# Optimization experiments

Hardware: AMD Instinct MI355X
Metric: run time of the kernel (lower is better)

## Reference

```python
import jax, jax.numpy as jnp
import numpy as np
import math

H, D, E, KD = 8, 128, 128, 16      # n_heads, input_dim, embed_dim, key_dim=val_dim
B, NPICK, NDEL = 16, 250, 250      # batch, pickups, deliveries per instance
G = 1 + NPICK + NDEL               # depot + picks + deliveries


def setup_inputs() -> dict:
    key = jax.random.key(0)
    ks = jax.random.split(key, 10)
    sk = 1.0 / math.sqrt(KD)
    se = 1.0 / math.sqrt(E)
    u = lambda k, shp, s: jax.random.uniform(k, shp, jnp.float32, -s, s)
    return {
        "q": jax.random.normal(ks[0], (B, G, D), jnp.float32),
        "W_query": u(ks[1], (H, D, KD), sk),
        "W_key": u(ks[2], (H, D, KD), sk),
        "W_val": u(ks[3], (H, D, KD), sk),
        "W1_query": u(ks[4], (H, D, KD), sk),
        "W2_query": u(ks[5], (H, D, KD), sk),
        "W3_query": u(ks[6], (H, D, KD), sk),
        "W4_query": u(ks[7], (H, D, KD), sk),
        "W_out": u(ks[8], (H, KD, E), se),
        "n_pick": NPICK,
        "n_delivery": NDEL,
    }


def reference(q, W_query, W_key, W_val, W1_query, W2_query, W3_query, W4_query,
              W_out, n_pick, n_delivery):
    h = q                                   # self-attention (h is None in caller)
    Bq, Gq, Dq = h.shape
    nh = W_query.shape[0]
    kd = W_query.shape[2]
    nf = 1.0 / math.sqrt(kd)
    NEG = jnp.float32(-jnp.inf)

    proj = lambda x, W: jnp.einsum('bnd,hdk->hbnk', x, W)   # (H,B,N,kd)
    scores = lambda Q, K: nf * jnp.einsum('hbqk,hbgk->hbqg', Q, K)
    # torch masked_fill_(x==0, -inf) on the group blocks (padding sentinel)
    zmask = lambda c: jnp.where(c == 0, NEG, c)

    Q = proj(q, W_query)
    K = proj(h, W_key)
    V = proj(h, W_val)
    comp = scores(Q, K)                      # (H,B,G,G)

    # split_embeddings: depot at 0, picks 1..n_pick, deliveries at the end
    hp = h[:, 1:1 + n_pick]                  # (B, n_pick, D)
    hd = h[:, 1 + n_pick:]                   # (B, n_delivery, D)

    Kp, Vp = proj(hp, W_key), proj(hp, W_val)
    Kd, Vd = proj(hd, W_key), proj(hd, W_val)

    c_pp = zmask(scores(proj(hp, W1_query), Kp))  # pick  -> all picks
    c_pd = zmask(scores(proj(hp, W2_query), Kd))  # pick  -> all deliveries
    c_dp = zmask(scores(proj(hd, W3_query), Kp))  # deliv -> all picks
    c_dd = zmask(scores(proj(hd, W4_query), Kd))  # deliv -> all deliveries

    def place(block, row_start):
        # scatter block rows into a (H,B,G,cols) tensor filled with -inf
        full = jnp.full((nh, Bq, Gq, block.shape[3]), NEG, dtype=block.dtype)
        return full.at[:, :, row_start:row_start + block.shape[2], :].set(block)

    add_pp = place(c_pp, 1)
    add_pd = place(c_pd, 1)
    add_dd = place(c_dd, Gq - n_delivery)
    add_dp = place(c_dp, Gq - n_delivery)

    comp_full = jnp.concatenate([comp, add_pp, add_pd, add_dd, add_dp], axis=-1)
    attn = jax.nn.softmax(comp_full, axis=-1)

    g, mp, md = Gq, n_pick, n_delivery
    heads = jnp.einsum('hbqg,hbgv->hbqv', attn[..., :g], V)
    heads = heads + jnp.einsum('hbqp,hbpv->hbqv', attn[..., g:g + mp], Vp)
    heads = heads + jnp.einsum('hbqd,hbdv->hbqv', attn[..., g + mp:g + mp + md], Vd)
    heads = heads + jnp.einsum('hbqd,hbdv->hbqv', attn[..., g + mp + md:g + mp + 2 * md], Vd)
    heads = heads + jnp.einsum('hbqp,hbpv->hbqv', attn[..., g + mp + 2 * md:g + 2 * mp + 2 * md], Vp)

    out = jnp.einsum('hbqv,hve->bqe', heads, W_out)   # (B, G, E)
    return out
```

## Files before the change

### kernel.cpp

```cpp
#include <hip/hip_runtime.h>
#include <math.h>

#define NH 8
#define DIM 128
#define KD 16
#define NB 16
#define NG 501
#define NPK 250
#define QROWS 512
#define QSCALE 0.36067376022224085f

typedef unsigned short ushort_t;
typedef __attribute__((ext_vector_type(8))) short short8v;
typedef __attribute__((ext_vector_type(4))) short short4v;
typedef __attribute__((ext_vector_type(2))) short short2v;
typedef __attribute__((ext_vector_type(4))) float f32x4;

#define MFMA(a, b, c) __builtin_amdgcn_mfma_f32_16x16x32_bf16(a, b, c, 0, 0, 0)

static __device__ __forceinline__ ushort_t f2bf(float x) {
  union { float f; unsigned u; } v; v.f = x;
  unsigned r = v.u + 0x7FFFu + ((v.u >> 16) & 1u);
  return (ushort_t)(r >> 16);
}
static __device__ __forceinline__ float bf2f(ushort_t h) {
  union { unsigned u; float f; } v; v.u = ((unsigned)h) << 16;
  return v.f;
}
static __device__ __forceinline__ unsigned cvtpk(float lo, float hi) {
  unsigned r;
  asm("v_cvt_pk_bf16_f32 %0, %1, %2" : "=v"(r) : "v"(lo), "v"(hi));
  return r;
}

__global__ __launch_bounds__(256) void conv_kernel(
    const float* __restrict__ q, ushort_t* __restrict__ qh,
    ushort_t* __restrict__ ql)
{
  int idx = blockIdx.x * 256 + threadIdx.x;
  int b  = idx >> 13;
  int r  = (idx >> 4) & 511;
  int c8 = (idx & 15) * 8;
  short8v h8 = {0,0,0,0,0,0,0,0}, l8 = {0,0,0,0,0,0,0,0};
  if (r < NG) {
    const float* src = &q[(size_t)(b * NG + r) * DIM + c8];
    float4 a = *(const float4*)src, d = *(const float4*)(src + 4);
    float vals[8] = {a.x, a.y, a.z, a.w, d.x, d.y, d.z, d.w};
#pragma unroll
    for (int j = 0; j < 8; ++j) {
      ushort_t hi = f2bf(vals[j]);
      h8[j] = (short)hi;
      l8[j] = (short)f2bf(vals[j] - bf2f(hi));
    }
  }
  size_t off = (size_t)(b * 512 + r) * DIM + c8;
  *(short8v*)&qh[off] = h8;
  *(short8v*)&ql[off] = l8;
}

__global__ __launch_bounds__(256) void proj_kernel(
    const ushort_t* __restrict__ qh_g, const ushort_t* __restrict__ ql_g,
    const float* __restrict__ wq, const float* __restrict__ wk,
    const float* __restrict__ wv, const float* __restrict__ w1,
    const float* __restrict__ w2, const float* __restrict__ w3,
    const float* __restrict__ w4,
    ushort_t* __restrict__ QcH, ushort_t* __restrict__ QcL,
    ushort_t* __restrict__ QPH, ushort_t* __restrict__ QPL,
    ushort_t* __restrict__ QDH, ushort_t* __restrict__ QDL,
    ushort_t* __restrict__ Kb,  ushort_t* __restrict__ Vt)
{
  const int rc = blockIdx.x, b = blockIdx.y, h = blockIdx.z;
  const int tid = threadIdx.x;
  const int wid = tid >> 6, lane = tid & 63;
  const int lrow = lane & 15, kgrp = lane >> 4;
  const size_t hb = (size_t)h * NB + b;

  const float* Wptr[7] = {wq, wk, wv, w1, w2, w3, w4};
  const int p0 = wid * 2;
  const int p1 = (wid < 3) ? wid * 2 + 1 : -1;

  short8v whf[2][4], wlf[2][4];
#pragma unroll
  for (int slot = 0; slot < 2; ++slot) {
    int p = slot ? p1 : p0;
    if (p < 0) continue;
    const float* W = Wptr[p] + h * 2048 + lrow;
#pragma unroll
    for (int c = 0; c < 4; ++c) {
      short8v hh, ll;
#pragma unroll
      for (int j = 0; j < 8; ++j) {
        float v = W[(c * 32 + kgrp * 8 + j) * 16];
        ushort_t hi = f2bf(v);
        hh[j] = (short)hi;
        ll[j] = (short)f2bf(v - bf2f(hi));
      }
      whf[slot][c] = hh; wlf[slot][c] = ll;
    }
  }

  const f32x4 zero4 = {0.f, 0.f, 0.f, 0.f};

#pragma unroll 1
  for (int iter = 0; iter < 2; ++iter) {
    const int rowbase = rc * 64 + iter * 32;
    short8v qhf[2][4], qlf[2][4];
#pragma unroll
    for (int s = 0; s < 2; ++s)
#pragma unroll
      for (int c = 0; c < 4; ++c) {
        size_t off = (size_t)(b * 512 + rowbase + s * 16 + lrow) * DIM + c * 32 + kgrp * 8;
        qhf[s][c] = *(const short8v*)(qh_g + off);
        qlf[s][c] = *(const short8v*)(ql_g + off);
      }

    f32x4 acc[2][2] = {{zero4, zero4}, {zero4, zero4}};
#pragma unroll
    for (int c = 0; c < 4; ++c)
#pragma unroll
      for (int slot = 0; slot < 2; ++slot) {
        int p = slot ? p1 : p0;
        if (p < 0) continue;
#pragma unroll
        for (int s = 0; s < 2; ++s) {
          if (p == 2) {
            acc[slot][s] = MFMA(whf[slot][c], qlf[s][c], acc[slot][s]);
            acc[slot][s] = MFMA(wlf[slot][c], qhf[s][c], acc[slot][s]);
            acc[slot][s] = MFMA(whf[slot][c], qhf[s][c], acc[slot][s]);
          } else {
            acc[slot][s] = MFMA(qlf[s][c], whf[slot][c], acc[slot][s]);
            acc[slot][s] = MFMA(qhf[s][c], wlf[slot][c], acc[slot][s]);
            acc[slot][s] = MFMA(qhf[s][c], whf[slot][c], acc[slot][s]);
          }
        }
      }

#pragma unroll
    for (int slot = 0; slot < 2; ++slot) {
      int p = slot ? p1 : p0;
      if (p < 0) continue;
#pragma unroll
      for (int s = 0; s < 2; ++s) {
#pragma unroll
        for (int rg = 0; rg < 4; ++rg) {
          float x = acc[slot][s][rg];
          if (p == 2) {
            int v = kgrp * 4 + rg;
            int g = rowbase + s * 16 + lrow;
            Vt[hb * 8192 + (size_t)v * 512 + g] = f2bf(x);
          } else {
            int row = rowbase + s * 16 + kgrp * 4 + rg;
            if (p == 0) {
              float xs = x * QSCALE;
              ushort_t hi = f2bf(xs), lo = f2bf(xs - bf2f(hi));
              size_t off = hb * 8192 + (size_t)row * 16 + lrow;
              QcH[off] = hi; QcL[off] = lo;
            } else if (p == 1) {
              ushort_t hi = f2bf(x), lo = f2bf(x - bf2f(hi));
              size_t off = hb * 16384 + (size_t)row * 32 + lrow;
              Kb[off] = hi; Kb[off + 16] = lo;
            } else {
              bool lowr = (p == 3 || p == 4);
              bool write = lowr ? (row <= NPK) : (row > NPK);
              if (write) {
                float xs = (row == 0) ? 0.f : x * QSCALE;
                ushort_t hi = f2bf(xs), lo = f2bf(xs - bf2f(hi));
                ushort_t* dH = (p == 3 || p == 5) ? QPH : QDH;
                ushort_t* dL = (p == 3 || p == 5) ? QPL : QDL;
                size_t off = hb * 8192 + (size_t)row * 16 + lrow;
                dH[off] = hi; dL[off] = lo;
              }
            }
          }
        }
      }
    }
  }
}

__global__ __launch_bounds__(256, 2) void attn_kernel(
    const ushort_t* __restrict__ QcH, const ushort_t* __restrict__ QcL,
    const ushort_t* __restrict__ QPH, const ushort_t* __restrict__ QPL,
    const ushort_t* __restrict__ QDH, const ushort_t* __restrict__ QDL,
    const ushort_t* __restrict__ Kb,  const ushort_t* __restrict__ Vt,
    ushort_t* __restrict__ HdH, ushort_t* __restrict__ HdL)
{
  __shared__ __align__(16) ushort_t Klds[16384];
  __shared__ __align__(16) ushort_t Vlds[8192];

  const int rt = blockIdx.x, b = blockIdx.y, h = blockIdx.z;
  const int tid = threadIdx.x;
  const int wid = tid >> 6, lane = tid & 63;
  const int lhalf = lane >> 4, lcol = lane & 15;
  const size_t hb = (size_t)h * NB + b;

  const ushort_t* Kg = Kb + hb * (size_t)(QROWS * 32);
  for (int c = tid; c < 2048; c += 256)
    *(short8v*)&Klds[c * 8] = *(const short8v*)(Kg + (size_t)c * 8);

  const ushort_t* Vg = Vt + hb * (size_t)(16 * QROWS);
#pragma unroll
  for (int it = 0; it < 4; ++it) {
    int c = it * 256 + tid;
    int blk = (it * 16) + (c & 15);
    int v = (c >> 4) & 15;
    int grp = blk >> 2, lh = blk & 3;
    short8v val = *(const short8v*)(Vg + (size_t)v * QROWS + blk * 8);
    *(short8v*)&Vlds[((grp * 4 + lh) * 16 + v) * 8] = val;
  }
  __syncthreads();

  const int wrow = rt * 128 + wid * 32;
  short8v qch[2], qcl[2], qph[2], qpl[2], qdh[2], qdl[2];
#pragma unroll
  for (int f = 0; f < 2; ++f) {
    int row = wrow + f * 16 + lcol;
    size_t off = hb * (size_t)(QROWS * 16) + (size_t)row * 16;
    size_t offh = off + (lhalf & 1) * 8;
    qch[f] = *(const short8v*)(QcH + offh);
    qph[f] = *(const short8v*)(QPH + offh);
    qdh[f] = *(const short8v*)(QDH + offh);
    short8v zl = {0,0,0,0,0,0,0,0};
    qcl[f] = zl; qpl[f] = zl; qdl[f] = zl;
    if (lhalf < 2) {
      size_t offl = off + lhalf * 8;
      qcl[f] = *(const short8v*)(QcL + offl);
      qpl[f] = *(const short8v*)(QPL + offl);
      qdl[f] = *(const short8v*)(QDL + offl);
    }
  }

  const f32x4 zero4 = {0.f, 0.f, 0.f, 0.f};
  f32x4 Oacc[2] = {zero4, zero4};
  float lsum[2] = {0.f, 0.f};
  const int srcA = ((lhalf & 1) * 2) * 16 + lcol;
  const int srcB = srcA + 16;
  const bool selhi = (lhalf >= 2);

#pragma unroll 1
  for (int grp = 0; grp < 16; ++grp) {
    float pv[2][2][4];
#pragma unroll
    for (int half = 0; half < 2; ++half) {
      const int ch = grp * 2 + half;
      short8v ka = *(const short8v*)&Klds[((ch * 16 + lcol) * 4 + lhalf) * 8];
#pragma unroll
      for (int qf = 0; qf < 2; ++qf) {
        f32x4 sc = MFMA(ka, qcl[qf], zero4);
        sc = MFMA(ka, qch[qf], sc);
        f32x4 se;
        if (ch == 15) {
          f32x4 sp = MFMA(ka, qpl[qf], zero4); sp = MFMA(ka, qph[qf], sp);
          f32x4 sd = MFMA(ka, qdl[qf], zero4); sd = MFMA(ka, qdh[qf], sd);
#pragma unroll
          for (int rg = 0; rg < 4; ++rg) {
            int key = 240 + lhalf * 4 + rg;
            se[rg] = (key <= NPK) ? sp[rg] : sd[rg];
          }
        } else if (ch <= 14) {
          se = MFMA(ka, qpl[qf], zero4); se = MFMA(ka, qph[qf], se);
        } else {
          se = MFMA(ka, qdl[qf], zero4); se = MFMA(ka, qdh[qf], se);
        }
#pragma unroll
        for (int rg = 0; rg < 4; ++rg) {
          float ec = __builtin_amdgcn_exp2f(sc[rg]);
          float ee = (se[rg] == 0.0f) ? 0.0f : __builtin_amdgcn_exp2f(se[rg]);
          if (ch == 0 && rg == 0) ee = (lhalf == 0) ? 0.0f : ee;
          float pt = ec + ee;
          if (ch == 31) pt = (lhalf * 4 + rg <= 4) ? pt : 0.0f;
          lsum[qf] += pt;
          pv[half][qf][rg] = pt;
        }
      }
    }
#pragma unroll
    for (int qf = 0; qf < 2; ++qf) {
      unsigned a0 = cvtpk(pv[0][qf][0], pv[0][qf][1]);
      unsigned a1 = cvtpk(pv[0][qf][2], pv[0][qf][3]);
      unsigned b0 = cvtpk(pv[1][qf][0], pv[1][qf][1]);
      unsigned b1 = cvtpk(pv[1][qf][2], pv[1][qf][3]);
      unsigned h0A = (unsigned)__shfl((int)a0, srcA);
      unsigned h0B = (unsigned)__shfl((int)a1, srcA);
      unsigned h0C = (unsigned)__shfl((int)a0, srcB);
      unsigned h0D = (unsigned)__shfl((int)a1, srcB);
      unsigned h1A = (unsigned)__shfl((int)b0, srcA);
      unsigned h1B = (unsigned)__shfl((int)b1, srcA);
      unsigned h1C = (unsigned)__shfl((int)b0, srcB);
      unsigned h1D = (unsigned)__shfl((int)b1, srcB);
      union { unsigned u[4]; short8v s; } pb;
      pb.u[0] = selhi ? h1A : h0A;
      pb.u[1] = selhi ? h1B : h0B;
      pb.u[2] = selhi ? h1C : h0C;
      pb.u[3] = selhi ? h1D : h0D;
      short8v va = *(const short8v*)&Vlds[((grp * 4 + lhalf) * 16 + lcol) * 8];
      Oacc[qf] = MFMA(va, pb.s, Oacc[qf]);
    }
  }

#pragma unroll
  for (int qf = 0; qf < 2; ++qf) {
    float l = lsum[qf];
    l += __shfl_xor(l, 16);
    l += __shfl_xor(l, 32);
    float inv = 1.0f / l;
    int row = wrow + qf * 16 + lcol;
    if (row < NG) {
      short4v ph, pl;
#pragma unroll
      for (int rg = 0; rg < 4; ++rg) {
        float o = Oacc[qf][rg] * inv;
        ushort_t hi = f2bf(o);
        ph[rg] = (short)hi;
        pl[rg] = (short)f2bf(o - bf2f(hi));
      }
      size_t off = (hb * 512 + (size_t)row) * 16 + lhalf * 4;
      *(short4v*)&HdH[off] = ph;
      *(short4v*)&HdL[off] = pl;
    }
  }
}

__global__ __launch_bounds__(256) void out_kernel(
    const ushort_t* __restrict__ HdH, const ushort_t* __restrict__ HdL,
    const float* __restrict__ Wout, float* __restrict__ out)
{
  const int eh = blockIdx.x, rt = blockIdx.y, b = blockIdx.z;
  const int tid = threadIdx.x;
  const int wid = tid >> 6, lane = tid & 63;
  const int lrow = lane & 15, kgrp = lane >> 4;
  const int e0 = eh * 64 + wid * 16 + lrow;

  short8v bh[4], bl[4];
#pragma unroll
  for (int c = 0; c < 4; ++c) {
    short8v hh, ll;
#pragma unroll
    for (int j = 0; j < 8; ++j) {
      float v = Wout[(size_t)(c * 32 + kgrp * 8 + j) * 128 + e0];
      ushort_t hi = f2bf(v);
      hh[j] = (short)hi;
      ll[j] = (short)f2bf(v - bf2f(hi));
    }
    bh[c] = hh; bl[c] = ll;
  }

  short8v ah[2][4], al[2][4];
#pragma unroll
  for (int s = 0; s < 2; ++s)
#pragma unroll
    for (int c = 0; c < 4; ++c) {
      int hh = (c * 4 + kgrp) >> 1, kd0 = ((c * 4 + kgrp) & 1) * 8;
      size_t off = ((size_t)(hh * NB + b) * 512 + rt * 32 + s * 16 + lrow) * 16 + kd0;
      ah[s][c] = *(const short8v*)(HdH + off);
      al[s][c] = *(const short8v*)(HdL + off);
    }

  const f32x4 zero4 = {0.f, 0.f, 0.f, 0.f};
  f32x4 acc[2] = {zero4, zero4};
#pragma unroll
  for (int c = 0; c < 4; ++c)
#pragma unroll
    for (int s = 0; s < 2; ++s) {
      acc[s] = MFMA(al[s][c], bh[c], acc[s]);
      acc[s] = MFMA(ah[s][c], bl[c], acc[s]);
      acc[s] = MFMA(ah[s][c], bh[c], acc[s]);
    }

#pragma unroll
  for (int s = 0; s < 2; ++s)
#pragma unroll
    for (int rg = 0; rg < 4; ++rg) {
      int g = rt * 32 + s * 16 + kgrp * 4 + rg;
      if (g < NG) out[((size_t)b * NG + g) * 128 + e0] = acc[s][rg];
    }
}

extern "C" void kernel_launch(void* const* d_in, const int* in_sizes, int n_in,
                              void* d_out, int out_size, void* d_ws, size_t ws_size,
                              hipStream_t stream)
{
  const float* q  = (const float*)d_in[0];
  const float* Wq = (const float*)d_in[1];
  const float* Wk = (const float*)d_in[2];
  const float* Wv = (const float*)d_in[3];
  const float* W1 = (const float*)d_in[4];
  const float* W2 = (const float*)d_in[5];
  const float* W3 = (const float*)d_in[6];
  const float* W4 = (const float*)d_in[7];
  const float* Wo = (const float*)d_in[8];
  float* out = (float*)d_out;

  char* wsb = (char*)d_ws;
  ushort_t* qh_g = (ushort_t*)(wsb + (0u  << 20));
  ushort_t* ql_g = (ushort_t*)(wsb + (2u  << 20));
  ushort_t* QcH  = (ushort_t*)(wsb + (4u  << 20));
  ushort_t* QcL  = (ushort_t*)(wsb + (6u  << 20));
  ushort_t* QPH  = (ushort_t*)(wsb + (8u  << 20));
  ushort_t* QPL  = (ushort_t*)(wsb + (10u << 20));
  ushort_t* QDH  = (ushort_t*)(wsb + (12u << 20));
  ushort_t* QDL  = (ushort_t*)(wsb + (14u << 20));
  ushort_t* Kb   = (ushort_t*)(wsb + (16u << 20));
  ushort_t* Vt   = (ushort_t*)(wsb + (20u << 20));
  ushort_t* HdH  = qh_g;
  ushort_t* HdL  = ql_g;

  conv_kernel<<<dim3(512), 256, 0, stream>>>(q, qh_g, ql_g);
  proj_kernel<<<dim3(8, NB, NH), 256, 0, stream>>>(qh_g, ql_g,
                                                   Wq, Wk, Wv, W1, W2, W3, W4,
                                                   QcH, QcL, QPH, QPL, QDH, QDL, Kb, Vt);
  attn_kernel<<<dim3(4, NB, NH), 256, 0, stream>>>(QcH, QcL, QPH, QPL, QDH, QDL,
                                                   Kb, Vt, HdH, HdL);
  out_kernel<<<dim3(2, 16, NB), 256, 0, stream>>>(HdH, HdL, Wo, out);
}
```

Baseline: 129.9 us.

## Pre-split weights once in conv kernel; shrink per-wave work in attn and out kernels

Moves the fp32-to-bf16 hi/lo splitting of all projection and output weights into the conversion kernel, writing them once in MFMA fragment layout instead of redoing the split in every proj and out block. The proj kernel now streams weights and q fragments per k-chunk to lower register pressure and raise occupancy. The attention kernel switches to 512-thread blocks where each wave handles 16 rows instead of 32, and the out kernel launches twice as many blocks with half the rows each. The aim is more parallelism and less redundant conversion, at the cost of extra workspace traffic and more K/V LDS loads per row.

```diff
diff --git a/kernel.cpp b/kernel.cpp
--- a/kernel.cpp
+++ b/kernel.cpp
@@ -13,7 +13,6 @@
 typedef unsigned short ushort_t;
 typedef __attribute__((ext_vector_type(8))) short short8v;
 typedef __attribute__((ext_vector_type(4))) short short4v;
-typedef __attribute__((ext_vector_type(2))) short short2v;
 typedef __attribute__((ext_vector_type(4))) float f32x4;
 
 #define MFMA(a, b, c) __builtin_amdgcn_mfma_f32_16x16x32_bf16(a, b, c, 0, 0, 0)
@@ -33,37 +32,61 @@
   return r;
 }
 
+
 __global__ __launch_bounds__(256) void conv_kernel(
-    const float* __restrict__ q, ushort_t* __restrict__ qh,
-    ushort_t* __restrict__ ql)
-{
-  int idx = blockIdx.x * 256 + threadIdx.x;
-  int b  = idx >> 13;
-  int r  = (idx >> 4) & 511;
-  int c8 = (idx & 15) * 8;
-  short8v h8 = {0,0,0,0,0,0,0,0}, l8 = {0,0,0,0,0,0,0,0};
-  if (r < NG) {
-    const float* src = &q[(size_t)(b * NG + r) * DIM + c8];
-    float4 a = *(const float4*)src, d = *(const float4*)(src + 4);
-    float vals[8] = {a.x, a.y, a.z, a.w, d.x, d.y, d.z, d.w};
-#pragma unroll
-    for (int j = 0; j < 8; ++j) {
-      ushort_t hi = f2bf(vals[j]);
-      h8[j] = (short)hi;
-      l8[j] = (short)f2bf(vals[j] - bf2f(hi));
-    }
-  }
-  size_t off = (size_t)(b * 512 + r) * DIM + c8;
-  *(short8v*)&qh[off] = h8;
-  *(short8v*)&ql[off] = l8;
-}
-
-__global__ __launch_bounds__(256) void proj_kernel(
-    const ushort_t* __restrict__ qh_g, const ushort_t* __restrict__ ql_g,
+    const float* __restrict__ q,
     const float* __restrict__ wq, const float* __restrict__ wk,
     const float* __restrict__ wv, const float* __restrict__ w1,
     const float* __restrict__ w2, const float* __restrict__ w3,
-    const float* __restrict__ w4,
+    const float* __restrict__ w4, const float* __restrict__ wo,
+    ushort_t* __restrict__ qh_g, ushort_t* __restrict__ ql_g,
+    ushort_t* __restrict__ Wsh,  ushort_t* __restrict__ Wsl,
+    ushort_t* __restrict__ Wosh, ushort_t* __restrict__ Wosl)
+{
+  const int idx = blockIdx.x * 256 + threadIdx.x;
+  {
+    int b = idx >> 13, r = (idx >> 4) & 511, c8 = (idx & 15) * 8;
+    short8v h8 = {0,0,0,0,0,0,0,0}, l8 = {0,0,0,0,0,0,0,0};
+    if (r < NG) {
+      const float* src = &q[(size_t)(b * NG + r) * DIM + c8];
+      float4 x = *(const float4*)src, y = *(const float4*)(src + 4);
+      float vals[8] = {x.x, x.y, x.z, x.w, y.x, y.y, y.z, y.w};
+#pragma unroll
+      for (int j = 0; j < 8; ++j) {
+        ushort_t hi = f2bf(vals[j]);
+        h8[j] = (short)hi;
+        l8[j] = (short)f2bf(vals[j] - bf2f(hi));
+      }
+    }
+    size_t off = (size_t)(b * 512 + r) * DIM + c8;
+    *(short8v*)&qh_g[off] = h8;
+    *(short8v*)&ql_g[off] = l8;
+  }
+  if (idx < 114688) {
+    int p = idx >> 14, rem = idx & 16383;
+    int h = rem >> 11, r2 = rem & 2047;
+    int d = r2 >> 4, lrow = r2 & 15;
+    const float* W = (p == 0) ? wq : (p == 1) ? wk : (p == 2) ? wv :
+                     (p == 3) ? w1 : (p == 4) ? w2 : (p == 5) ? w3 : w4;
+    float v = W[h * 2048 + d * 16 + lrow];
+    ushort_t hi = f2bf(v), lo = f2bf(v - bf2f(hi));
+    int c = d >> 5, kg = (d >> 3) & 3, j = d & 7;
+    size_t dst = ((((size_t)(p * 8 + h) * 4 + c) * 4 + kg) * 16 + lrow) * 8 + j;
+    Wsh[dst] = hi; Wsl[dst] = lo;
+  }
+  if (idx < 16384) {
+    int hkd = idx >> 7, e = idx & 127;
+    float v = wo[(size_t)hkd * 128 + e];
+    ushort_t hi = f2bf(v), lo = f2bf(v - bf2f(hi));
+    int c = hkd >> 5, kg = (hkd >> 3) & 3, j = hkd & 7;
+    size_t dst = (((size_t)c * 4 + kg) * 128 + e) * 8 + j;
+    Wosh[dst] = hi; Wosl[dst] = lo;
+  }
+}
+
+__global__ __launch_bounds__(256, 4) void proj_kernel(
+    const ushort_t* __restrict__ qh_g, const ushort_t* __restrict__ ql_g,
+    const ushort_t* __restrict__ Wsh,  const ushort_t* __restrict__ Wsl,
     ushort_t* __restrict__ QcH, ushort_t* __restrict__ QcL,
     ushort_t* __restrict__ QPH, ushort_t* __restrict__ QPL,
     ushort_t* __restrict__ QDH, ushort_t* __restrict__ QDL,
@@ -74,66 +97,46 @@
   const int wid = tid >> 6, lane = tid & 63;
   const int lrow = lane & 15, kgrp = lane >> 4;
   const size_t hb = (size_t)h * NB + b;
-
-  const float* Wptr[7] = {wq, wk, wv, w1, w2, w3, w4};
   const int p0 = wid * 2;
   const int p1 = (wid < 3) ? wid * 2 + 1 : -1;
-
-  short8v whf[2][4], wlf[2][4];
-#pragma unroll
-  for (int slot = 0; slot < 2; ++slot) {
-    int p = slot ? p1 : p0;
-    if (p < 0) continue;
-    const float* W = Wptr[p] + h * 2048 + lrow;
-#pragma unroll
-    for (int c = 0; c < 4; ++c) {
-      short8v hh, ll;
-#pragma unroll
-      for (int j = 0; j < 8; ++j) {
-        float v = W[(c * 32 + kgrp * 8 + j) * 16];
-        ushort_t hi = f2bf(v);
-        hh[j] = (short)hi;
-        ll[j] = (short)f2bf(v - bf2f(hi));
-      }
-      whf[slot][c] = hh; wlf[slot][c] = ll;
-    }
-  }
-
   const f32x4 zero4 = {0.f, 0.f, 0.f, 0.f};
 
 #pragma unroll 1
   for (int iter = 0; iter < 2; ++iter) {
     const int rowbase = rc * 64 + iter * 32;
-    short8v qhf[2][4], qlf[2][4];
-#pragma unroll
-    for (int s = 0; s < 2; ++s)
-#pragma unroll
-      for (int c = 0; c < 4; ++c) {
-        size_t off = (size_t)(b * 512 + rowbase + s * 16 + lrow) * DIM + c * 32 + kgrp * 8;
-        qhf[s][c] = *(const short8v*)(qh_g + off);
-        qlf[s][c] = *(const short8v*)(ql_g + off);
-      }
-
     f32x4 acc[2][2] = {{zero4, zero4}, {zero4, zero4}};
 #pragma unroll
-    for (int c = 0; c < 4; ++c)
+    for (int c = 0; c < 4; ++c) {
+      size_t qoff0 = (size_t)(b * 512 + rowbase + lrow) * DIM + c * 32 + kgrp * 8;
+      size_t qoff1 = qoff0 + 16 * DIM;
+      short8v qh0 = *(const short8v*)(qh_g + qoff0);
+      short8v ql0 = *(const short8v*)(ql_g + qoff0);
+      short8v qh1 = *(const short8v*)(qh_g + qoff1);
+      short8v ql1 = *(const short8v*)(ql_g + qoff1);
 #pragma unroll
       for (int slot = 0; slot < 2; ++slot) {
         int p = slot ? p1 : p0;
         if (p < 0) continue;
-#pragma unroll
-        for (int s = 0; s < 2; ++s) {
-          if (p == 2) {
-            acc[slot][s] = MFMA(whf[slot][c], qlf[s][c], acc[slot][s]);
-            acc[slot][s] = MFMA(wlf[slot][c], qhf[s][c], acc[slot][s]);
-            acc[slot][s] = MFMA(whf[slot][c], qhf[s][c], acc[slot][s]);
-          } else {
-            acc[slot][s] = MFMA(qlf[s][c], whf[slot][c], acc[slot][s]);
-            acc[slot][s] = MFMA(qhf[s][c], wlf[slot][c], acc[slot][s]);
-            acc[slot][s] = MFMA(qhf[s][c], whf[slot][c], acc[slot][s]);
-          }
+        size_t woff = ((((size_t)(p * 8 + h) * 4 + c) * 4 + kgrp) * 16 + lrow) * 8;
+        short8v wh = *(const short8v*)&Wsh[woff];
+        short8v wl = *(const short8v*)&Wsl[woff];
+        if (p == 2) {
+          acc[slot][0] = MFMA(wh, ql0, acc[slot][0]);
+          acc[slot][0] = MFMA(wl, qh0, acc[slot][0]);
+          acc[slot][0] = MFMA(wh, qh0, acc[slot][0]);
+          acc[slot][1] = MFMA(wh, ql1, acc[slot][1]);
+          acc[slot][1] = MFMA(wl, qh1, acc[slot][1]);
+          acc[slot][1] = MFMA(wh, qh1, acc[slot][1]);
+        } else {
+          acc[slot][0] = MFMA(ql0, wh, acc[slot][0]);
+          acc[slot][0] = MFMA(qh0, wl, acc[slot][0]);
+          acc[slot][0] = MFMA(qh0, wh, acc[slot][0]);
+          acc[slot][1] = MFMA(ql1, wh, acc[slot][1]);
+          acc[slot][1] = MFMA(qh1, wl, acc[slot][1]);
+          acc[slot][1] = MFMA(qh1, wh, acc[slot][1]);
         }
       }
+    }
 
 #pragma unroll
     for (int slot = 0; slot < 2; ++slot) {
@@ -178,7 +181,7 @@
   }
 }
 
-__global__ __launch_bounds__(256, 2) void attn_kernel(
+__global__ __launch_bounds__(512, 4) void attn_kernel(
     const ushort_t* __restrict__ QcH, const ushort_t* __restrict__ QcL,
     const ushort_t* __restrict__ QPH, const ushort_t* __restrict__ QPL,
     const ushort_t* __restrict__ QDH, const ushort_t* __restrict__ QDL,
@@ -194,186 +197,159 @@
   const int lhalf = lane >> 4, lcol = lane & 15;
   const size_t hb = (size_t)h * NB + b;
 
+  const int wrow = rt * 128 + wid * 16;
+  const int row = wrow + lcol;
+  size_t off = hb * (size_t)(QROWS * 16) + (size_t)row * 16;
+  size_t offh = off + (lhalf & 1) * 8;
+  short8v qch = *(const short8v*)(QcH + offh);
+  short8v qph = *(const short8v*)(QPH + offh);
+  short8v qdh = *(const short8v*)(QDH + offh);
+  short8v qcl = {0,0,0,0,0,0,0,0}, qpl = qcl, qdl = qcl;
+  if (lhalf < 2) {
+    size_t offl = off + lhalf * 8;
+    qcl = *(const short8v*)(QcL + offl);
+    qpl = *(const short8v*)(QPL + offl);
+    qdl = *(const short8v*)(QDL + offl);
+  }
+
   const ushort_t* Kg = Kb + hb * (size_t)(QROWS * 32);
-  for (int c = tid; c < 2048; c += 256)
+  for (int c = tid; c < 2048; c += 512)
     *(short8v*)&Klds[c * 8] = *(const short8v*)(Kg + (size_t)c * 8);
-
   const ushort_t* Vg = Vt + hb * (size_t)(16 * QROWS);
 #pragma unroll
-  for (int it = 0; it < 4; ++it) {
-    int c = it * 256 + tid;
-    int blk = (it * 16) + (c & 15);
-    int v = (c >> 4) & 15;
-    int grp = blk >> 2, lh = blk & 3;
+  for (int it = 0; it < 2; ++it) {
+    int i = it * 512 + tid;
+    int v = (i >> 4) & 15;
+    int blk = (i >> 8) * 16 + (i & 15);
+    int g2 = blk >> 2, lh = blk & 3;
     short8v val = *(const short8v*)(Vg + (size_t)v * QROWS + blk * 8);
-    *(short8v*)&Vlds[((grp * 4 + lh) * 16 + v) * 8] = val;
+    *(short8v*)&Vlds[((g2 * 4 + lh) * 16 + v) * 8] = val;
   }
   __syncthreads();
 
-  const int wrow = rt * 128 + wid * 32;
-  short8v qch[2], qcl[2], qph[2], qpl[2], qdh[2], qdl[2];
-#pragma unroll
-  for (int f = 0; f < 2; ++f) {
-    int row = wrow + f * 16 + lcol;
-    size_t off = hb * (size_t)(QROWS * 16) + (size_t)row * 16;
-    size_t offh = off + (lhalf & 1) * 8;
-    qch[f] = *(const short8v*)(QcH + offh);
-    qph[f] = *(const short8v*)(QPH + offh);
-    qdh[f] = *(const short8v*)(QDH + offh);
-    short8v zl = {0,0,0,0,0,0,0,0};
-    qcl[f] = zl; qpl[f] = zl; qdl[f] = zl;
-    if (lhalf < 2) {
-      size_t offl = off + lhalf * 8;
-      qcl[f] = *(const short8v*)(QcL + offl);
-      qpl[f] = *(const short8v*)(QPL + offl);
-      qdl[f] = *(const short8v*)(QDL + offl);
-    }
-  }
-
   const f32x4 zero4 = {0.f, 0.f, 0.f, 0.f};
-  f32x4 Oacc[2] = {zero4, zero4};
-  float lsum[2] = {0.f, 0.f};
+  f32x4 Oacc = zero4;
+  float lsum = 0.f;
   const int srcA = ((lhalf & 1) * 2) * 16 + lcol;
   const int srcB = srcA + 16;
   const bool selhi = (lhalf >= 2);
 
 #pragma unroll 1
   for (int grp = 0; grp < 16; ++grp) {
-    float pv[2][2][4];
+    const int ch0 = grp * 2, ch1 = ch0 + 1;
+    short8v ka0 = *(const short8v*)&Klds[((ch0 * 16 + lcol) * 4 + lhalf) * 8];
+    short8v ka1 = *(const short8v*)&Klds[((ch1 * 16 + lcol) * 4 + lhalf) * 8];
+    short8v va  = *(const short8v*)&Vlds[((grp * 4 + lhalf) * 16 + lcol) * 8];
+
+    float pv[2][4];
 #pragma unroll
     for (int half = 0; half < 2; ++half) {
-      const int ch = grp * 2 + half;
-      short8v ka = *(const short8v*)&Klds[((ch * 16 + lcol) * 4 + lhalf) * 8];
-#pragma unroll
-      for (int qf = 0; qf < 2; ++qf) {
-        f32x4 sc = MFMA(ka, qcl[qf], zero4);
-        sc = MFMA(ka, qch[qf], sc);
-        f32x4 se;
-        if (ch == 15) {
-          f32x4 sp = MFMA(ka, qpl[qf], zero4); sp = MFMA(ka, qph[qf], sp);
-          f32x4 sd = MFMA(ka, qdl[qf], zero4); sd = MFMA(ka, qdh[qf], sd);
-#pragma unroll
-          for (int rg = 0; rg < 4; ++rg) {
-            int key = 240 + lhalf * 4 + rg;
-            se[rg] = (key <= NPK) ? sp[rg] : sd[rg];
-          }
-        } else if (ch <= 14) {
-          se = MFMA(ka, qpl[qf], zero4); se = MFMA(ka, qph[qf], se);
-        } else {
-          se = MFMA(ka, qdl[qf], zero4); se = MFMA(ka, qdh[qf], se);
+      const int ch = ch0 + half;
+      short8v ka = half ? ka1 : ka0;
+      f32x4 sc = MFMA(ka, qcl, zero4);
+      sc = MFMA(ka, qch, sc);
+      f32x4 se;
+      if (ch == 15) {
+        f32x4 sp = MFMA(ka, qpl, zero4); sp = MFMA(ka, qph, sp);
+        f32x4 sd = MFMA(ka, qdl, zero4); sd = MFMA(ka, qdh, sd);
+#pragma unroll
+        for (int rg = 0; rg < 4; ++rg) {
+          int key = 240 + lhalf * 4 + rg;
+          se[rg] = (key <= NPK) ? sp[rg] : sd[rg];
         }
-#pragma unroll
-        for (int rg = 0; rg < 4; ++rg) {
-          float ec = __builtin_amdgcn_exp2f(sc[rg]);
-          float ee = (se[rg] == 0.0f) ? 0.0f : __builtin_amdgcn_exp2f(se[rg]);
-          if (ch == 0 && rg == 0) ee = (lhalf == 0) ? 0.0f : ee;
-          float pt = ec + ee;
-          if (ch == 31) pt = (lhalf * 4 + rg <= 4) ? pt : 0.0f;
-          lsum[qf] += pt;
-          pv[half][qf][rg] = pt;
-        }
-      }
-    }
-#pragma unroll
-    for (int qf = 0; qf < 2; ++qf) {
-      unsigned a0 = cvtpk(pv[0][qf][0], pv[0][qf][1]);
-      unsigned a1 = cvtpk(pv[0][qf][2], pv[0][qf][3]);
-      unsigned b0 = cvtpk(pv[1][qf][0], pv[1][qf][1]);
-      unsigned b1 = cvtpk(pv[1][qf][2], pv[1][qf][3]);
-      unsigned h0A = (unsigned)__shfl((int)a0, srcA);
-      unsigned h0B = (unsigned)__shfl((int)a1, srcA);
-      unsigned h0C = (unsigned)__shfl((int)a0, srcB);
-      unsigned h0D = (unsigned)__shfl((int)a1, srcB);
-      unsigned h1A = (unsigned)__shfl((int)b0, srcA);
-      unsigned h1B = (unsigned)__shfl((int)b1, srcA);
-      unsigned h1C = (unsigned)__shfl((int)b0, srcB);
-      unsigned h1D = (unsigned)__shfl((int)b1, srcB);
-      union { unsigned u[4]; short8v s; } pb;
-      pb.u[0] = selhi ? h1A : h0A;
-      pb.u[1] = selhi ? h1B : h0B;
-      pb.u[2] = selhi ? h1C : h0C;
-      pb.u[3] = selhi ? h1D : h0D;
-      short8v va = *(const short8v*)&Vlds[((grp * 4 + lhalf) * 16 + lcol) * 8];
-      Oacc[qf] = MFMA(va, pb.s, Oacc[qf]);
-    }
-  }
-
-#pragma unroll
-  for (int qf = 0; qf < 2; ++qf) {
-    float l = lsum[qf];
-    l += __shfl_xor(l, 16);
-    l += __shfl_xor(l, 32);
-    float inv = 1.0f / l;
-    int row = wrow + qf * 16 + lcol;
-    if (row < NG) {
-      short4v ph, pl;
+      } else if (ch <= 14) {
+        se = MFMA(ka, qpl, zero4); se = MFMA(ka, qph, se);
+      } else {
+        se = MFMA(ka, qdl, zero4); se = MFMA(ka, qdh, se);
+      }
 #pragma unroll
       for (int rg = 0; rg < 4; ++rg) {
-        float o = Oacc[qf][rg] * inv;
-        ushort_t hi = f2bf(o);
-        ph[rg] = (short)hi;
-        pl[rg] = (short)f2bf(o - bf2f(hi));
-      }
-      size_t off = (hb * 512 + (size_t)row) * 16 + lhalf * 4;
-      *(short4v*)&HdH[off] = ph;
-      *(short4v*)&HdL[off] = pl;
-    }
-  }
-}
-
-__global__ __launch_bounds__(256) void out_kernel(
+        float ec = __builtin_amdgcn_exp2f(sc[rg]);
+        float ee = (se[rg] == 0.0f) ? 0.0f : __builtin_amdgcn_exp2f(se[rg]);
+        if (ch == 0 && rg == 0) ee = (lhalf == 0) ? 0.0f : ee;
+        float pt = ec + ee;
+        if (ch == 31) pt = (lhalf * 4 + rg <= 4) ? pt : 0.0f;
+        lsum += pt;
+        pv[half][rg] = pt;
+      }
+    }
+    unsigned a0 = cvtpk(pv[0][0], pv[0][1]);
+    unsigned a1 = cvtpk(pv[0][2], pv[0][3]);
+    unsigned b0 = cvtpk(pv[1][0], pv[1][1]);
+    unsigned b1 = cvtpk(pv[1][2], pv[1][3]);
+    unsigned h0A = (unsigned)__shfl((int)a0, srcA);
+    unsigned h0B = (unsigned)__shfl((int)a1, srcA);
+    unsigned h0C = (unsigned)__shfl((int)a0, srcB);
+    unsigned h0D = (unsigned)__shfl((int)a1, srcB);
+    unsigned h1A = (unsigned)__shfl((int)b0, srcA);
+    unsigned h1B = (unsigned)__shfl((int)b1, srcA);
+    unsigned h1C = (unsigned)__shfl((int)b0, srcB);
+    unsigned h1D = (unsigned)__shfl((int)b1, srcB);
+    union { unsigned u[4]; short8v s; } pb;
+    pb.u[0] = selhi ? h1A : h0A;
+    pb.u[1] = selhi ? h1B : h0B;
+    pb.u[2] = selhi ? h1C : h0C;
+    pb.u[3] = selhi ? h1D : h0D;
+    Oacc = MFMA(va, pb.s, Oacc);
+  }
+
+  float l = lsum;
+  l += __shfl_xor(l, 16);
+  l += __shfl_xor(l, 32);
+  float inv = 1.0f / l;
+  if (row < NG) {
+    short4v ph, pl;
+#pragma unroll
+    for (int rg = 0; rg < 4; ++rg) {
+      float o = Oacc[rg] * inv;
+      ushort_t hi = f2bf(o);
+      ph[rg] = (short)hi;
+      pl[rg] = (short)f2bf(o - bf2f(hi));
+    }
+    size_t doff = (hb * 512 + (size_t)row) * 16 + lhalf * 4;
+    *(short4v*)&HdH[doff] = ph;
+    *(short4v*)&HdL[doff] = pl;
+  }
+}
+
+__global__ __launch_bounds__(256, 4) void out_kernel(
     const ushort_t* __restrict__ HdH, const ushort_t* __restrict__ HdL,
-    const float* __restrict__ Wout, float* __restrict__ out)
-{
-  const int eh = blockIdx.x, rt = blockIdx.y, b = blockIdx.z;
+    const ushort_t* __restrict__ Wosh, const ushort_t* __restrict__ Wosl,
+    float* __restrict__ out)
+{
+  const int eh = blockIdx.x >> 1, s = blockIdx.x & 1;
+  const int rt = blockIdx.y, b = blockIdx.z;
   const int tid = threadIdx.x;
   const int wid = tid >> 6, lane = tid & 63;
   const int lrow = lane & 15, kgrp = lane >> 4;
   const int e0 = eh * 64 + wid * 16 + lrow;
 
-  short8v bh[4], bl[4];
+  short8v bh[4], bl[4], ah[4], al[4];
 #pragma unroll
   for (int c = 0; c < 4; ++c) {
-    short8v hh, ll;
-#pragma unroll
-    for (int j = 0; j < 8; ++j) {
-      float v = Wout[(size_t)(c * 32 + kgrp * 8 + j) * 128 + e0];
-      ushort_t hi = f2bf(v);
-      hh[j] = (short)hi;
-      ll[j] = (short)f2bf(v - bf2f(hi));
-    }
-    bh[c] = hh; bl[c] = ll;
-  }
-
-  short8v ah[2][4], al[2][4];
-#pragma unroll
-  for (int s = 0; s < 2; ++s)
-#pragma unroll
-    for (int c = 0; c < 4; ++c) {
-      int hh = (c * 4 + kgrp) >> 1, kd0 = ((c * 4 + kgrp) & 1) * 8;
-      size_t off = ((size_t)(hh * NB + b) * 512 + rt * 32 + s * 16 + lrow) * 16 + kd0;
-      ah[s][c] = *(const short8v*)(HdH + off);
-      al[s][c] = *(const short8v*)(HdL + off);
-    }
+    size_t boff = (((size_t)c * 4 + kgrp) * 128 + e0) * 8;
+    bh[c] = *(const short8v*)&Wosh[boff];
+    bl[c] = *(const short8v*)&Wosl[boff];
+    int hh = (c * 4 + kgrp) >> 1, kd0 = ((c * 4 + kgrp) & 1) * 8;
+    size_t aoff = ((size_t)(hh * NB + b) * 512 + rt * 32 + s * 16 + lrow) * 16 + kd0;
+    ah[c] = *(const short8v*)(HdH + aoff);
+    al[c] = *(const short8v*)(HdL + aoff);
+  }
 
   const f32x4 zero4 = {0.f, 0.f, 0.f, 0.f};
-  f32x4 acc[2] = {zero4, zero4};
-#pragma unroll
-  for (int c = 0; c < 4; ++c)
-#pragma unroll
-    for (int s = 0; s < 2; ++s) {
-      acc[s] = MFMA(al[s][c], bh[c], acc[s]);
-      acc[s] = MFMA(ah[s][c], bl[c], acc[s]);
-      acc[s] = MFMA(ah[s][c], bh[c], acc[s]);
-    }
-
-#pragma unroll
-  for (int s = 0; s < 2; ++s)
-#pragma unroll
-    for (int rg = 0; rg < 4; ++rg) {
-      int g = rt * 32 + s * 16 + kgrp * 4 + rg;
-      if (g < NG) out[((size_t)b * NG + g) * 128 + e0] = acc[s][rg];
-    }
+  f32x4 acc = zero4;
+#pragma unroll
+  for (int c = 0; c < 4; ++c) {
+    acc = MFMA(al[c], bh[c], acc);
+    acc = MFMA(ah[c], bl[c], acc);
+    acc = MFMA(ah[c], bh[c], acc);
+  }
+
+#pragma unroll
+  for (int rg = 0; rg < 4; ++rg) {
+    int g = rt * 32 + s * 16 + kgrp * 4 + rg;
+    if (g < NG) out[((size_t)b * NG + g) * 128 + e0] = acc[rg];
+  }
 }
 
 extern "C" void kernel_launch(void* const* d_in, const int* in_sizes, int n_in,
@@ -402,14 +378,18 @@
   ushort_t* QDL  = (ushort_t*)(wsb + (14u << 20));
   ushort_t* Kb   = (ushort_t*)(wsb + (16u << 20));
   ushort_t* Vt   = (ushort_t*)(wsb + (20u << 20));
+  ushort_t* Wsh  = (ushort_t*)(wsb + (22u << 20));
+  ushort_t* Wsl  = (ushort_t*)(wsb + (23u << 20));
+  ushort_t* Wosh = (ushort_t*)(wsb + (24u << 20));
+  ushort_t* Wosl = (ushort_t*)(wsb + (25u << 20));
   ushort_t* HdH  = qh_g;
   ushort_t* HdL  = ql_g;
 
-  conv_kernel<<<dim3(512), 256, 0, stream>>>(q, qh_g, ql_g);
-  proj_kernel<<<dim3(8, NB, NH), 256, 0, stream>>>(qh_g, ql_g,
-                                                   Wq, Wk, Wv, W1, W2, W3, W4,
+  conv_kernel<<<dim3(512), 256, 0, stream>>>(q, Wq, Wk, Wv, W1, W2, W3, W4, Wo,
+                                             qh_g, ql_g, Wsh, Wsl, Wosh, Wosl);
+  proj_kernel<<<dim3(8, NB, NH), 256, 0, stream>>>(qh_g, ql_g, Wsh, Wsl,
                                                    QcH, QcL, QPH, QPL, QDH, QDL, Kb, Vt);
-  attn_kernel<<<dim3(4, NB, NH), 256, 0, stream>>>(QcH, QcL, QPH, QPL, QDH, QDL,
-                                                   Kb, Vt, HdH, HdL);
-  out_kernel<<<dim3(2, 16, NB), 256, 0, stream>>>(HdH, HdL, Wo, out);
-}
+  attn_kernel<<<dim3(4, NB, NH), dim3(512), 0, stream>>>(QcH, QcL, QPH, QPL, QDH, QDL,
+                                                         Kb, Vt, HdH, HdL);
+  out_kernel<<<dim3(4, 16, NB), 256, 0, stream>>>(HdH, HdL, Wosh, Wosl, out);
+}
```

Measured after the change: 124.6 us. 4.1% less time.
